# Performance work log

Measured on AMD Instinct MI355X. Metric: run time of the kernel, lower is better.

Reference implementation:

```python
import jax, jax.numpy as jnp
import numpy as np

CONTACT_THRESHOLD = 0.5
DEFAULT_LEN = 0.1
EPS = 1e-6


def _orthonormalize(m):
    # Gram-Schmidt on rows -> proper rotation matrices, vectorized over leading dims
    a1 = m[..., 0, :]
    a2 = m[..., 1, :]
    b1 = a1 / jnp.linalg.norm(a1, axis=-1, keepdims=True)
    a2p = a2 - jnp.sum(b1 * a2, axis=-1, keepdims=True) * b1
    b2 = a2p / jnp.linalg.norm(a2p, axis=-1, keepdims=True)
    b3 = jnp.cross(b1, b2)
    return jnp.stack([b1, b2, b3], axis=-2)


def setup_inputs() -> dict:
    key = jax.random.key(0)
    k1, k2, k3, k4 = jax.random.split(key, 4)
    B, T = 512, 4096
    pred_hand_contact_prob = jax.random.uniform(k1, (B, T, 2), dtype=jnp.float32)
    pred_hand_positions = jax.random.normal(k2, (B, T, 2, 3), dtype=jnp.float32)
    obj_rotm = _orthonormalize(jax.random.normal(k3, (B, T, 3, 3), dtype=jnp.float32))
    obj_trans_init = jax.random.normal(k4, (B, 3), dtype=jnp.float32)
    return {
        'pred_hand_contact_prob': pred_hand_contact_prob,
        'pred_hand_positions': pred_hand_positions,
        'obj_rotm': obj_rotm,
        'obj_trans_init': obj_trans_init,
    }


def _fk_obj_trans(contact_prob, hand_pos, obj_rotm, obj_trans_init):
    B, T, _ = contact_prob.shape
    dtype = hand_pos.dtype
    lc = contact_prob[..., 0] > CONTACT_THRESHOLD  # [B,T]
    rc = contact_prob[..., 1] > CONTACT_THRESHOLD
    t0 = jnp.zeros((B, 1), bool)  # frame 0 forced no-contact
    ls = jnp.concatenate([t0, lc[:, 1:] & ~lc[:, :-1]], axis=1)
    rs = jnp.concatenate([t0, rc[:, 1:] & ~rc[:, :-1]], axis=1)
    lc = jnp.concatenate([t0, lc[:, 1:]], axis=1)
    rc = jnp.concatenate([t0, rc[:, 1:]], axis=1)
    z_unit = jnp.array([0.0, 0.0, 1.0], dtype=dtype)
    bidx = jnp.arange(B)

    def step(carry, xs):
        current, obj_pos, dir_local, dist = carry  # [B] int32, [B,3], [B,3], [B]
        l_c, r_c, l_s, r_s, hands, R = xs  # hands [B,2,3], R [B,3,3]
        new = jnp.where(l_s, 0, jnp.where(r_s, 1, -1))
        has_contact = ((current == 0) & l_c) | ((current == 1) & r_c)
        has_other = ((current == 0) & r_c) | ((current == 1) & l_c)
        grab = (new != -1) | (~has_contact & has_other)
        cur_grab = jnp.where(new != -1, new, 1 - current)
        release = ~grab & ~has_contact & (current != -1)
        new_current = jnp.where(grab, cur_grab, jnp.where(release, -1, current))
        # grab: recompute local direction + distance from previous obj_pos
        hand0 = hands[bidx, jnp.clip(cur_grab, 0, 1)]  # [B,3]
        vec = obj_pos - hand0
        d0 = jnp.linalg.norm(vec, axis=-1)
        valid = d0 > EPS
        unit = jnp.where(valid[:, None], vec / jnp.maximum(d0, EPS)[:, None], z_unit)
        d0 = jnp.where(valid, d0, jnp.asarray(DEFAULT_LEN, dtype))
        dir_new = jnp.einsum('bij,bi->bj', R, unit)  # R^T @ unit
        dir_local = jnp.where(grab[:, None], dir_new, dir_local)
        dist = jnp.where(grab, d0, dist)
        # attached: obj_pos = hand + R @ dir_local * dist
        attached = new_current != -1
        hand_cur = hands[bidx, jnp.clip(new_current, 0, 1)]
        new_pos = hand_cur + jnp.einsum('bij,bj->bi', R, dir_local) * dist[:, None]
        obj_pos = jnp.where(attached[:, None], new_pos, obj_pos)
        return (new_current, obj_pos, dir_local, dist), obj_pos

    carry0 = (jnp.full((B,), -1, jnp.int32),
              obj_trans_init.astype(dtype),
              jnp.zeros((B, 3), dtype),
              jnp.zeros((B,), dtype))
    xs = (lc.T, rc.T, ls.T, rs.T,
          jnp.swapaxes(hand_pos, 0, 1),
          jnp.swapaxes(obj_rotm, 0, 1))
    _, out = jax.lax.scan(step, carry0, xs)  # out [T,B,3]
    return jnp.swapaxes(out, 0, 1)  # [B,T,3]


def reference(pred_hand_contact_prob, pred_hand_positions, obj_rotm, obj_trans_init):
    return _fk_obj_trans(pred_hand_contact_prob, pred_hand_positions, obj_rotm, obj_trans_init)
```

## Files before the change

### kernel.cpp

```cpp
#include <hip/hip_runtime.h>


#define FSM_ID 0x24

__device__ __forceinline__ int fsm_compose(int f, int g) {
    int r0 = (f >> (((g     ) & 3) << 1)) & 3;
    int r1 = (f >> (((g >> 2) & 3) << 1)) & 3;
    int r2 = (f >> (((g >> 4) & 3) << 1)) & 3;
    return r0 | (r1 << 2) | (r2 << 4);
}

__device__ __forceinline__ void tmap_identity(float* m, int& rp, int& rw) {
    #pragma unroll
    for (int i = 0; i < 24; ++i) m[i] = 0.f;
    m[0] = m[4] = m[8] = 1.f;
    m[12] = m[16] = m[20] = 1.f;
    rp = 0; rw = 1;
}

__device__ __forceinline__ void tmap_compose(
    const float* Lm, int Lrp, int Lrw,
    const float* Em, int Erp, int Erw,
    float* Om, int& Orp, int& Orw)
{
    {
        float EM[9], Ec[3];
        #pragma unroll
        for (int i = 0; i < 9; ++i) EM[i] = Lrp ? Em[12+i] : Em[i];
        #pragma unroll
        for (int i = 0; i < 3; ++i) Ec[i] = Lrp ? Em[21+i] : Em[9+i];
        #pragma unroll
        for (int i = 0; i < 3; ++i) {
            #pragma unroll
            for (int j = 0; j < 3; ++j)
                Om[3*i+j] = Lm[3*i]*EM[j] + Lm[3*i+1]*EM[3+j] + Lm[3*i+2]*EM[6+j];
            Om[9+i] = Lm[3*i]*Ec[0] + Lm[3*i+1]*Ec[1] + Lm[3*i+2]*Ec[2] + Lm[9+i];
        }
        Orp = Lrp ? Erw : Erp;
    }
    {
        float EM[9], Ec[3];
        #pragma unroll
        for (int i = 0; i < 9; ++i) EM[i] = Lrw ? Em[12+i] : Em[i];
        #pragma unroll
        for (int i = 0; i < 3; ++i) Ec[i] = Lrw ? Em[21+i] : Em[9+i];
        #pragma unroll
        for (int i = 0; i < 3; ++i) {
            #pragma unroll
            for (int j = 0; j < 3; ++j)
                Om[12+3*i+j] = Lm[12+3*i]*EM[j] + Lm[12+3*i+1]*EM[3+j] + Lm[12+3*i+2]*EM[6+j];
            Om[21+i] = Lm[12+3*i]*Ec[0] + Lm[12+3*i+1]*Ec[1] + Lm[12+3*i+2]*Ec[2] + Lm[21+i];
        }
        Orw = Lrw ? Erw : Erp;
    }
}

__device__ __forceinline__ void tmap_apply(
    const float* m, int rp_, int rw_,
    const float* pin, const float* win, float* pout, float* wout)
{
    const float* ip = rp_ ? win : pin;
    pout[0] = m[0]*ip[0] + m[1]*ip[1] + m[2]*ip[2] + m[9];
    pout[1] = m[3]*ip[0] + m[4]*ip[1] + m[5]*ip[2] + m[10];
    pout[2] = m[6]*ip[0] + m[7]*ip[1] + m[8]*ip[2] + m[11];
    const float* iw = rw_ ? win : pin;
    wout[0] = m[12]*iw[0] + m[13]*iw[1] + m[14]*iw[2] + m[21];
    wout[1] = m[15]*iw[0] + m[16]*iw[1] + m[17]*iw[2] + m[22];
    wout[2] = m[18]*iw[0] + m[19]*iw[1] + m[20]*iw[2] + m[23];
}

__global__ __launch_bounds__(1024) void fk_scan_par5(
    const float* __restrict__ prob,
    const float* __restrict__ hands,
    const float* __restrict__ rotm,
    const float* __restrict__ tinit,
    float* __restrict__ out)
{
    const int b    = blockIdx.x;
    const int c    = threadIdx.x;
    const int lane = c & 63;
    const int w    = c >> 6;

    __shared__ int   sFSM[16];
    __shared__ float sAm[16][24];
    __shared__ int   sAf[16];

    const float* prB = prob  + (size_t)b * 4096 * 2;
    const float* hdB = hands + (size_t)b * 4096 * 6;
    const float* rmB = rotm  + (size_t)b * 4096 * 9;
    float*       obB = out   + (size_t)b * 4096 * 3;

    const float4* pr4 = (const float4*)prB + c * 2;
    const float4* hd4 = (const float4*)hdB + c * 6;
    const float4* rm4 = (const float4*)rmB + c * 9;
    float4*       ob4 = (float4*)obB       + c * 3;

    unsigned lcB = 0, rcB = 0;
    #pragma unroll
    for (int i = 0; i < 2; ++i) {
        float4 v = pr4[i];
        lcB |= (unsigned)(v.x > 0.5f) << (2*i);
        rcB |= (unsigned)(v.y > 0.5f) << (2*i);
        lcB |= (unsigned)(v.z > 0.5f) << (2*i+1);
        rcB |= (unsigned)(v.w > 0.5f) << (2*i+1);
    }
    unsigned pL = 0, pR = 0;
    if (c) {
        float2 pv = *(const float2*)(prB + 8*c - 2);
        pL = pv.x > 0.5f ? 1u : 0u;
        pR = pv.y > 0.5f ? 1u : 0u;
    }
    unsigned lsB = lcB & ~((lcB << 1) | pL);
    unsigned rsB = rcB & ~((rcB << 1) | pR);
    if (c == 0) { lcB &= ~1u; rcB &= ~1u; lsB &= ~1u; rsB &= ~1u; }

    int M = FSM_ID;
    #pragma unroll
    for (int k = 0; k < 4; ++k) {
        const unsigned lc = (lcB >> k) & 1u, rc = (rcB >> k) & 1u;
        const unsigned ls = (lsB >> k) & 1u, rs = (rsB >> k) & 1u;
        const int nwi = (int)(ls | rs);
        const int nwe = ls ? 1 : 2;
        const int e0  = lc ? 1 : (rc ? 2 : 0);
        const int e1  = rc ? 2 : (lc ? 1 : 0);
        const int mt  = nwi ? nwe * 0x15 : ((e0 << 2) | (e1 << 4));
        M = fsm_compose(mt, M);
    }
    #pragma unroll
    for (int d = 1; d < 64; d <<= 1) {
        int v  = __shfl_up(M, d);
        int cc = fsm_compose(M, v);
        M = (lane >= d) ? cc : M;
    }
    if (lane == 63) sFSM[w] = M;
    __syncthreads();
    int Pf = FSM_ID;
    for (int i = 0; i < w; ++i) Pf = fsm_compose(sFSM[i], Pf);
    int Me = __shfl_up(M, 1);
    if (lane == 0) Me = FSM_ID;
    const int s_in = fsm_compose(Me, Pf) & 3;

    float Am[24]; int rp, rw;
    tmap_identity(Am, rp, rw);
    int s = s_in;
    {
        float rb[36], hb[24];
        #pragma unroll
        for (int j = 0; j < 9; ++j) {
            float4 v = rm4[j];
            rb[4*j]=v.x; rb[4*j+1]=v.y; rb[4*j+2]=v.z; rb[4*j+3]=v.w;
        }
        #pragma unroll
        for (int j = 0; j < 6; ++j) {
            float4 v = hd4[j];
            hb[4*j]=v.x; hb[4*j+1]=v.y; hb[4*j+2]=v.z; hb[4*j+3]=v.w;
        }
        #pragma unroll
        for (int k = 0; k < 4; ++k) {
            const unsigned lc=(lcB>>k)&1u, rc=(rcB>>k)&1u;
            const unsigned ls=(lsB>>k)&1u, rs=(rsB>>k)&1u;
            const int nwi  = (int)(ls|rs);
            const int c1 = (s==1), c2 = (s==2);
            const int hasc = (c1&(int)lc)|(c2&(int)rc);
            const int haso = (c1&(int)rc)|(c2&(int)lc);
            const int grab = nwi | ((hasc^1)&haso);
            const int gi   = nwi ? (ls?0:1) : c1;
            const int new_s= grab ? gi+1 : (hasc ? s : 0);
            const float* Rk = rb + 9*k;
            const float* Hk = hb + 6*k;
            if (grab) {
                const float hx = gi?Hk[3]:Hk[0], hy = gi?Hk[4]:Hk[1], hz = gi?Hk[5]:Hk[2];
                float t[9];
                #pragma unroll
                for (int i2=0;i2<3;++i2)
                    #pragma unroll
                    for (int j2=0;j2<3;++j2)
                        t[3*i2+j2] = Rk[i2]*Am[j2] + Rk[3+i2]*Am[3+j2] + Rk[6+i2]*Am[6+j2];
                const float ex=Am[9]-hx, ey=Am[10]-hy, ez=Am[11]-hz;
                Am[21] = Rk[0]*ex + Rk[3]*ey + Rk[6]*ez;
                Am[22] = Rk[1]*ex + Rk[4]*ey + Rk[7]*ez;
                Am[23] = Rk[2]*ex + Rk[5]*ey + Rk[8]*ez;
                #pragma unroll
                for (int i2=0;i2<9;++i2) Am[12+i2] = t[i2];
                rw = rp;
            } else if (new_s) {
                const int ci = new_s - 1;
                const float hx = ci?Hk[3]:Hk[0], hy = ci?Hk[4]:Hk[1], hz = ci?Hk[5]:Hk[2];
                float t[9];
                #pragma unroll
                for (int i2=0;i2<3;++i2)
                    #pragma unroll
                    for (int j2=0;j2<3;++j2)
                        t[3*i2+j2] = Rk[3*i2]*Am[12+j2] + Rk[3*i2+1]*Am[15+j2] + Rk[3*i2+2]*Am[18+j2];
                const float e0_ = hx + Rk[0]*Am[21] + Rk[1]*Am[22] + Rk[2]*Am[23];
                const float e1_ = hy + Rk[3]*Am[21] + Rk[4]*Am[22] + Rk[5]*Am[23];
                const float e2_ = hz + Rk[6]*Am[21] + Rk[7]*Am[22] + Rk[8]*Am[23];
                #pragma unroll
                for (int i2=0;i2<9;++i2) Am[i2] = t[i2];
                Am[9]=e0_; Am[10]=e1_; Am[11]=e2_;
                rp = rw;
            }
            s = new_s;
        }
    }

    #pragma unroll 1
    for (int d = 1; d < 64; d <<= 1) {
        float Em[24];
        #pragma unroll
        for (int i = 0; i < 24; ++i) Em[i] = __shfl_up(Am[i], d);
        const int Ef = __shfl_up(rp | (rw<<1), d);
        float Om[24]; int orp, orw;
        tmap_compose(Am, rp, rw, Em, Ef&1, (Ef>>1)&1, Om, orp, orw);
        const bool act = (lane >= d);
        #pragma unroll
        for (int i = 0; i < 24; ++i) Am[i] = act ? Om[i] : Am[i];
        rp = act ? orp : rp;
        rw = act ? orw : rw;
    }
    if (lane == 63) {
        #pragma unroll
        for (int i = 0; i < 24; ++i) sAm[w][i] = Am[i];
        sAf[w] = rp | (rw<<1);
    }
    __syncthreads();

    {
        #pragma unroll
        for (int i = 0; i < 24; ++i) Am[i] = __shfl_up(Am[i], 1);
        const int t = __shfl_up(rp | (rw<<1), 1);
        int nrp = t & 1, nrw = (t >> 1) & 1;
        if (lane == 0) tmap_identity(Am, nrp, nrw);
        rp = nrp; rw = nrw;
        if (lane == 0) { rp = 0; rw = 1; }
    }

    float vp[3] = { tinit[3*b], tinit[3*b+1], tinit[3*b+2] };
    float vw[3] = { 0.f, 0.f, 0.f };
    for (int i = 0; i < w; ++i) {
        float np[3], nw2[3];
        const int f = sAf[i];
        tmap_apply(&sAm[i][0], f & 1, (f >> 1) & 1, vp, vw, np, nw2);
        vp[0]=np[0]; vp[1]=np[1]; vp[2]=np[2];
        vw[0]=nw2[0]; vw[1]=nw2[1]; vw[2]=nw2[2];
    }
    float pv[3], wv[3];
    tmap_apply(Am, rp, rw, vp, vw, pv, wv);
    float px = pv[0], py = pv[1], pz = pv[2];
    float Wx = wv[0], Wy = wv[1], Wz = wv[2];

    s = s_in;
    {
        float rb[36], hb[24];
        #pragma unroll
        for (int j = 0; j < 9; ++j) {
            float4 v = rm4[j];
            rb[4*j]=v.x; rb[4*j+1]=v.y; rb[4*j+2]=v.z; rb[4*j+3]=v.w;
        }
        #pragma unroll
        for (int j = 0; j < 6; ++j) {
            float4 v = hd4[j];
            hb[4*j]=v.x; hb[4*j+1]=v.y; hb[4*j+2]=v.z; hb[4*j+3]=v.w;
        }
        float o[12];
        #pragma unroll
        for (int k = 0; k < 4; ++k) {
            const unsigned lc=(lcB>>k)&1u, rc=(rcB>>k)&1u;
            const unsigned ls=(lsB>>k)&1u, rs=(rsB>>k)&1u;
            const int nwi  = (int)(ls|rs);
            const int c1 = (s==1), c2 = (s==2);
            const int hasc = (c1&(int)lc)|(c2&(int)rc);
            const int haso = (c1&(int)rc)|(c2&(int)lc);
            const int grab = nwi | ((hasc^1)&haso);
            const int gi   = nwi ? (ls?0:1) : c1;
            const int new_s= grab ? gi+1 : (hasc ? s : 0);
            const float* Rk = rb + 9*k;
            const float* Hk = hb + 6*k;
            if (grab) {
                const float hx = gi?Hk[3]:Hk[0], hy = gi?Hk[4]:Hk[1], hz = gi?Hk[5]:Hk[2];
                const float vx = px-hx, vy = py-hy, vz = pz-hz;
                const float d2 = vx*vx + vy*vy + vz*vz;
                if (d2 > 1e-12f) {
                    Wx = Rk[0]*vx + Rk[3]*vy + Rk[6]*vz;
                    Wy = Rk[1]*vx + Rk[4]*vy + Rk[7]*vz;
                    Wz = Rk[2]*vx + Rk[5]*vy + Rk[8]*vz;
                } else {
                    Wx = 0.1f*Rk[6]; Wy = 0.1f*Rk[7]; Wz = 0.1f*Rk[8];
                }
            }
            if (new_s) {
                const int ci = new_s - 1;
                const float hx = ci?Hk[3]:Hk[0], hy = ci?Hk[4]:Hk[1], hz = ci?Hk[5]:Hk[2];
                px = hx + Rk[0]*Wx + Rk[1]*Wy + Rk[2]*Wz;
                py = hy + Rk[3]*Wx + Rk[4]*Wy + Rk[5]*Wz;
                pz = hz + Rk[6]*Wx + Rk[7]*Wy + Rk[8]*Wz;
            }
            s = new_s;
            o[3*k+0]=px; o[3*k+1]=py; o[3*k+2]=pz;
        }
        ob4[0] = make_float4(o[0], o[1], o[2],  o[3]);
        ob4[1] = make_float4(o[4], o[5], o[6],  o[7]);
        ob4[2] = make_float4(o[8], o[9], o[10], o[11]);
    }
}

#define CT 256
__global__ __launch_bounds__(64) void fk_scan_wave(
    const float* __restrict__ prob, const float* __restrict__ hands,
    const float* __restrict__ rotm, const float* __restrict__ tinit,
    float* __restrict__ out, int B, int T)
{
    __shared__ __align__(16) float sP[CT * 2];
    __shared__ __align__(16) float sH[CT * 8];
    __shared__ __align__(16) float sR[CT * 12];
    const int b = blockIdx.x, lane = threadIdx.x;
    const float* prB = prob  + (size_t)b * T * 2;
    const float* hdB = hands + (size_t)b * T * 6;
    const float* rmB = rotm  + (size_t)b * T * 9;
    float*       obB = out   + (size_t)b * T * 3;
    float px = tinit[3*b+0], py = tinit[3*b+1], pz = tinit[3*b+2];
    float Wx = 0.f, Wy = 0.f, Wz = 0.f;
    int cur = -1, prev_l = 0, prev_r = 0;
    for (int t0 = 0; t0 < T; t0 += CT) {
        const int n = (T - t0 < CT) ? (T - t0) : CT;
        for (int i = lane; i < n * 2; i += 64) sP[i] = prB[(size_t)t0*2 + i];
        for (int i = lane; i < n * 6; i += 64) {
            int s2 = i / 6, cc = i - 6*s2; sH[8*s2+cc] = hdB[(size_t)t0*6 + i];
        }
        for (int i = lane; i < n * 9; i += 64) {
            int s2 = i / 9, cc = i - 9*s2; sR[12*s2+cc] = rmB[(size_t)t0*9 + i];
        }
        __syncthreads();
        for (int k = 0; k < n; ++k) {
            const int t = t0 + k;
            const int rl = __builtin_amdgcn_readfirstlane(sP[2*k]   > 0.5f ? 1 : 0);
            const int rr = __builtin_amdgcn_readfirstlane(sP[2*k+1] > 0.5f ? 1 : 0);
            const int nz = (t != 0) ? 1 : 0;
            const int l_c = rl & nz, r_c = rr & nz;
            const int l_s = rl & (prev_l ^ 1) & nz, r_s = rr & (prev_r ^ 1) & nz;
            prev_l = rl; prev_r = rr;
            const int nw = l_s ? 0 : (r_s ? 1 : -1);
            const int hasc = ((cur==0)&l_c) | ((cur==1)&r_c);
            const int haso = ((cur==0)&r_c) | ((cur==1)&l_c);
            const int grab = (nw != -1) | ((hasc^1)&haso);
            const int new_cur = grab ? ((nw!=-1)?nw:(1-cur))
                                     : (((hasc^1)&(cur!=-1)) ? -1 : cur);
            if (new_cur != -1) {
                const float h0x=sH[8*k+0],h0y=sH[8*k+1],h0z=sH[8*k+2];
                const float h1x=sH[8*k+3],h1y=sH[8*k+4],h1z=sH[8*k+5];
                const float R0=sR[12*k+0],R1=sR[12*k+1],R2=sR[12*k+2];
                const float R3=sR[12*k+3],R4=sR[12*k+4],R5=sR[12*k+5];
                const float R6=sR[12*k+6],R7=sR[12*k+7],R8=sR[12*k+8];
                const float hx = new_cur ? h1x : h0x;
                const float hy = new_cur ? h1y : h0y;
                const float hz = new_cur ? h1z : h0z;
                if (grab) {
                    const float vx=px-hx, vy=py-hy, vz=pz-hz;
                    const float d2 = vx*vx+vy*vy+vz*vz;
                    if (d2 > 1e-12f) {
                        Wx = R0*vx+R3*vy+R6*vz; Wy = R1*vx+R4*vy+R7*vz; Wz = R2*vx+R5*vy+R8*vz;
                    } else { Wx = 0.1f*R6; Wy = 0.1f*R7; Wz = 0.1f*R8; }
                }
                px = hx + (R0*Wx+R1*Wy+R2*Wz);
                py = hy + (R3*Wx+R4*Wy+R5*Wz);
                pz = hz + (R6*Wx+R7*Wy+R8*Wz);
            }
            cur = new_cur;
            if (lane == 0) {
                obB[3*(size_t)t+0]=px; obB[3*(size_t)t+1]=py; obB[3*(size_t)t+2]=pz;
            }
        }
        __syncthreads();
    }
}

extern "C" void kernel_launch(void* const* d_in, const int* in_sizes, int n_in,
                              void* d_out, int out_size, void* d_ws, size_t ws_size,
                              hipStream_t stream) {
    const float* prob  = (const float*)d_in[0];
    const float* hands = (const float*)d_in[1];
    const float* rotm  = (const float*)d_in[2];
    const float* tinit = (const float*)d_in[3];
    float* out = (float*)d_out;

    const int B = in_sizes[3] / 3;
    const int T = in_sizes[0] / (B * 2);

    if (T == 4096) {
        hipLaunchKernelGGL(fk_scan_par5, dim3(B), dim3(1024), 0, stream,
                           prob, hands, rotm, tinit, out);
    } else {
        hipLaunchKernelGGL(fk_scan_wave, dim3(B), dim3(64), 0, stream,
                           prob, hands, rotm, tinit, out, B, T);
    }
}
```

Measured before the change: 61.71 us.

## Replace serial cross-wave prefix loops with a parallel 16-lane wave scan

The cross-wave carry for both the FSM state and the affine transform maps was previously built by each wave looping serially over all earlier waves' aggregates from shared memory. Now wave 0 runs a 16-lane shuffle scan over the wave aggregates once and writes per-wave starting states to shared memory, which every wave reads after an extra barrier. Each lane then applies its own inclusive map and takes the exclusive result via a shuffle. This removes up to 15 serial compose/apply steps per wave, in exchange for two extra __syncthreads and some register save/restore in wave 0.

```diff
diff --git a/kernel.cpp b/kernel.cpp
--- a/kernel.cpp
+++ b/kernel.cpp
@@ -69,7 +69,7 @@
     wout[2] = m[18]*iw[0] + m[19]*iw[1] + m[20]*iw[2] + m[23];
 }
 
-__global__ __launch_bounds__(1024) void fk_scan_par5(
+__global__ __launch_bounds__(1024) void fk_scan_par6(
     const float* __restrict__ prob,
     const float* __restrict__ hands,
     const float* __restrict__ rotm,
@@ -82,8 +82,12 @@
     const int w    = c >> 6;
 
     __shared__ int   sFSM[16];
+    __shared__ int   sSin[16];
     __shared__ float sAm[16][24];
     __shared__ int   sAf[16];
+    __shared__ float sSt[16][6];
+    __shared__ float sSave[16][24];
+    __shared__ int   sSvT[16];
 
     const float* prB = prob  + (size_t)b * 4096 * 2;
     const float* hdB = hands + (size_t)b * 4096 * 6;
@@ -134,11 +138,23 @@
     }
     if (lane == 63) sFSM[w] = M;
     __syncthreads();
-    int Pf = FSM_ID;
-    for (int i = 0; i < w; ++i) Pf = fsm_compose(sFSM[i], Pf);
+
+    if (w == 0 && lane < 16) {
+        int K = sFSM[lane];
+        #pragma unroll
+        for (int d = 1; d < 16; d <<= 1) {
+            int v  = __shfl_up(K, d);
+            int cc = fsm_compose(K, v);
+            K = (lane >= d) ? cc : K;
+        }
+        if (lane < 15) sSin[lane + 1] = K & 3;
+        if (lane == 0) sSin[0] = 0;
+    }
+    __syncthreads();
+
     int Me = __shfl_up(M, 1);
     if (lane == 0) Me = FSM_ID;
-    const int s_in = fsm_compose(Me, Pf) & 3;
+    const int s_in = (Me >> (2 * sSin[w])) & 3;
 
     float Am[24]; int rp, rw;
     tmap_identity(Am, rp, rw);
@@ -223,31 +239,63 @@
         for (int i = 0; i < 24; ++i) sAm[w][i] = Am[i];
         sAf[w] = rp | (rw<<1);
     }
+    if (w == 0 && lane < 16) {
+        #pragma unroll
+        for (int i = 0; i < 24; ++i) sSave[lane][i] = Am[i];
+        sSvT[lane] = rp | (rw<<1);
+    }
     __syncthreads();
 
-    {
-        #pragma unroll
-        for (int i = 0; i < 24; ++i) Am[i] = __shfl_up(Am[i], 1);
-        const int t = __shfl_up(rp | (rw<<1), 1);
-        int nrp = t & 1, nrw = (t >> 1) & 1;
-        if (lane == 0) tmap_identity(Am, nrp, nrw);
-        rp = nrp; rw = nrw;
-        if (lane == 0) { rp = 0; rw = 1; }
-    }
-
-    float vp[3] = { tinit[3*b], tinit[3*b+1], tinit[3*b+2] };
-    float vw[3] = { 0.f, 0.f, 0.f };
-    for (int i = 0; i < w; ++i) {
-        float np[3], nw2[3];
-        const int f = sAf[i];
-        tmap_apply(&sAm[i][0], f & 1, (f >> 1) & 1, vp, vw, np, nw2);
-        vp[0]=np[0]; vp[1]=np[1]; vp[2]=np[2];
-        vw[0]=nw2[0]; vw[1]=nw2[1]; vw[2]=nw2[2];
-    }
-    float pv[3], wv[3];
-    tmap_apply(Am, rp, rw, vp, vw, pv, wv);
-    float px = pv[0], py = pv[1], pz = pv[2];
-    float Wx = wv[0], Wy = wv[1], Wz = wv[2];
+    if (w == 0 && lane < 16) {
+        float Km[24];
+        #pragma unroll
+        for (int i = 0; i < 24; ++i) Km[i] = sAm[lane][i];
+        int kf = sAf[lane];
+        int krp = kf & 1, krw = (kf >> 1) & 1;
+        #pragma unroll 1
+        for (int d = 1; d < 16; d <<= 1) {
+            float Ek[24];
+            #pragma unroll
+            for (int i = 0; i < 24; ++i) Ek[i] = __shfl_up(Km[i], d);
+            const int Ef = __shfl_up(krp | (krw << 1), d);
+            float Ok[24]; int okp, okw;
+            tmap_compose(Km, krp, krw, Ek, Ef & 1, (Ef >> 1) & 1, Ok, okp, okw);
+            const bool act = (lane >= d);
+            #pragma unroll
+            for (int i = 0; i < 24; ++i) Km[i] = act ? Ok[i] : Km[i];
+            krp = act ? okp : krp;
+            krw = act ? okw : krw;
+        }
+        const float p0[3]  = { tinit[3*b], tinit[3*b+1], tinit[3*b+2] };
+        const float w0v[3] = { 0.f, 0.f, 0.f };
+        float sp[3], sw[3];
+        tmap_apply(Km, krp, krw, p0, w0v, sp, sw);
+        if (lane < 15) {
+            sSt[lane+1][0]=sp[0]; sSt[lane+1][1]=sp[1]; sSt[lane+1][2]=sp[2];
+            sSt[lane+1][3]=sw[0]; sSt[lane+1][4]=sw[1]; sSt[lane+1][5]=sw[2];
+        }
+        if (lane == 0) {
+            sSt[0][0]=p0[0]; sSt[0][1]=p0[1]; sSt[0][2]=p0[2];
+            sSt[0][3]=0.f;   sSt[0][4]=0.f;   sSt[0][5]=0.f;
+        }
+        #pragma unroll
+        for (int i = 0; i < 24; ++i) Am[i] = sSave[lane][i];
+        const int t2 = sSvT[lane];
+        rp = t2 & 1; rw = (t2 >> 1) & 1;
+    }
+    __syncthreads();
+
+    float vpv[3] = { sSt[w][0], sSt[w][1], sSt[w][2] };
+    float vwv[3] = { sSt[w][3], sSt[w][4], sSt[w][5] };
+    float ipv[3], iwv[3];
+    tmap_apply(Am, rp, rw, vpv, vwv, ipv, iwv);
+    float px = __shfl_up(ipv[0], 1);
+    float py = __shfl_up(ipv[1], 1);
+    float pz = __shfl_up(ipv[2], 1);
+    float Wx = __shfl_up(iwv[0], 1);
+    float Wy = __shfl_up(iwv[1], 1);
+    float Wz = __shfl_up(iwv[2], 1);
+    if (lane == 0) { px=vpv[0]; py=vpv[1]; pz=vpv[2]; Wx=vwv[0]; Wy=vwv[1]; Wz=vwv[2]; }
 
     s = s_in;
     {
@@ -387,7 +435,7 @@
     const int T = in_sizes[0] / (B * 2);
 
     if (T == 4096) {
-        hipLaunchKernelGGL(fk_scan_par5, dim3(B), dim3(1024), 0, stream,
+        hipLaunchKernelGGL(fk_scan_par6, dim3(B), dim3(1024), 0, stream,
                            prob, hands, rotm, tinit, out);
     } else {
         hipLaunchKernelGGL(fk_scan_wave, dim3(B), dim3(64), 0, stream,
```

New measurement: 63.95 us. 3.6% more time.

## Represent scan transform maps as quaternion plus translation in wave scan

Applied to the files above, without the earlier changes.

Each thread's local composed affine map, two 3x3 rotations plus offsets, is converted to a unit quaternion plus translation before the wave-level prefix scan. This cuts the per-step shuffle payload from 24 to 14 floats and uses cheaper quaternion products in place of 3x3 matrix multiplies. The exclusive-prefix step now shuffles the three-float applied result after applying the inclusive map, not the whole map. The trade-off is the cost of mat2quat conversions with branches and sqrt, plus rounding differences, and it assumes the composed matrices remain proper rotations.

```diff
diff --git a/kernel.cpp b/kernel.cpp
--- a/kernel.cpp
+++ b/kernel.cpp
@@ -10,66 +10,95 @@
     return r0 | (r1 << 2) | (r2 << 4);
 }
 
-__device__ __forceinline__ void tmap_identity(float* m, int& rp, int& rw) {
-    #pragma unroll
-    for (int i = 0; i < 24; ++i) m[i] = 0.f;
-    m[0] = m[4] = m[8] = 1.f;
-    m[12] = m[16] = m[20] = 1.f;
-    rp = 0; rw = 1;
-}
-
-__device__ __forceinline__ void tmap_compose(
-    const float* Lm, int Lrp, int Lrw,
-    const float* Em, int Erp, int Erw,
-    float* Om, int& Orp, int& Orw)
+__device__ __forceinline__ void qmul(const float* a, const float* b, float* o) {
+    o[0] = a[0]*b[0] - a[1]*b[1] - a[2]*b[2] - a[3]*b[3];
+    o[1] = a[0]*b[1] + a[1]*b[0] + a[2]*b[3] - a[3]*b[2];
+    o[2] = a[0]*b[2] - a[1]*b[3] + a[2]*b[0] + a[3]*b[1];
+    o[3] = a[0]*b[3] + a[1]*b[2] - a[2]*b[1] + a[3]*b[0];
+}
+
+__device__ __forceinline__ void qrot(const float* q, const float* v, float* o) {
+    const float ux = q[2]*v[2] - q[3]*v[1];
+    const float uy = q[3]*v[0] - q[1]*v[2];
+    const float uz = q[1]*v[1] - q[2]*v[0];
+    const float tx = ux + q[0]*v[0];
+    const float ty = uy + q[0]*v[1];
+    const float tz = uz + q[0]*v[2];
+    o[0] = fmaf(2.f, q[2]*tz - q[3]*ty, v[0]);
+    o[1] = fmaf(2.f, q[3]*tx - q[1]*tz, v[1]);
+    o[2] = fmaf(2.f, q[1]*ty - q[2]*tx, v[2]);
+}
+
+__device__ __forceinline__ void mat2quat(const float* m, float* q) {
+    const float tr = m[0] + m[4] + m[8];
+    float qw, qx, qy, qz;
+    if (tr > 0.f) {
+        const float S = sqrtf(tr + 1.0f) * 2.f, iS = 1.f / S;
+        qw = 0.25f * S;
+        qx = (m[7] - m[5]) * iS;
+        qy = (m[2] - m[6]) * iS;
+        qz = (m[3] - m[1]) * iS;
+    } else if (m[0] > m[4] && m[0] > m[8]) {
+        const float S = sqrtf(1.0f + m[0] - m[4] - m[8]) * 2.f, iS = 1.f / S;
+        qw = (m[7] - m[5]) * iS;
+        qx = 0.25f * S;
+        qy = (m[1] + m[3]) * iS;
+        qz = (m[2] + m[6]) * iS;
+    } else if (m[4] > m[8]) {
+        const float S = sqrtf(1.0f + m[4] - m[0] - m[8]) * 2.f, iS = 1.f / S;
+        qw = (m[2] - m[6]) * iS;
+        qx = (m[1] + m[3]) * iS;
+        qy = 0.25f * S;
+        qz = (m[5] + m[7]) * iS;
+    } else {
+        const float S = sqrtf(1.0f + m[8] - m[0] - m[4]) * 2.f, iS = 1.f / S;
+        qw = (m[3] - m[1]) * iS;
+        qx = (m[2] + m[6]) * iS;
+        qy = (m[5] + m[7]) * iS;
+        qz = 0.25f * S;
+    }
+    const float n = rsqrtf(qw*qw + qx*qx + qy*qy + qz*qz);
+    q[0] = qw*n; q[1] = qx*n; q[2] = qy*n; q[3] = qz*n;
+}
+
+__device__ __forceinline__ void qmap_compose(
+    const float* L, int Lrp, int Lrw,
+    const float* E, int Erp, int Erw,
+    float* O, int& Orp, int& Orw)
 {
-    {
-        float EM[9], Ec[3];
-        #pragma unroll
-        for (int i = 0; i < 9; ++i) EM[i] = Lrp ? Em[12+i] : Em[i];
-        #pragma unroll
-        for (int i = 0; i < 3; ++i) Ec[i] = Lrp ? Em[21+i] : Em[9+i];
-        #pragma unroll
-        for (int i = 0; i < 3; ++i) {
-            #pragma unroll
-            for (int j = 0; j < 3; ++j)
-                Om[3*i+j] = Lm[3*i]*EM[j] + Lm[3*i+1]*EM[3+j] + Lm[3*i+2]*EM[6+j];
-            Om[9+i] = Lm[3*i]*Ec[0] + Lm[3*i+1]*Ec[1] + Lm[3*i+2]*Ec[2] + Lm[9+i];
-        }
-        Orp = Lrp ? Erw : Erp;
-    }
-    {
-        float EM[9], Ec[3];
-        #pragma unroll
-        for (int i = 0; i < 9; ++i) EM[i] = Lrw ? Em[12+i] : Em[i];
-        #pragma unroll
-        for (int i = 0; i < 3; ++i) Ec[i] = Lrw ? Em[21+i] : Em[9+i];
-        #pragma unroll
-        for (int i = 0; i < 3; ++i) {
-            #pragma unroll
-            for (int j = 0; j < 3; ++j)
-                Om[12+3*i+j] = Lm[12+3*i]*EM[j] + Lm[12+3*i+1]*EM[3+j] + Lm[12+3*i+2]*EM[6+j];
-            Om[21+i] = Lm[12+3*i]*Ec[0] + Lm[12+3*i+1]*Ec[1] + Lm[12+3*i+2]*Ec[2] + Lm[21+i];
-        }
-        Orw = Lrw ? Erw : Erp;
-    }
-}
-
-__device__ __forceinline__ void tmap_apply(
+    float eq[4], ec[3], r[3];
+    #pragma unroll
+    for (int i = 0; i < 4; ++i) eq[i] = Lrp ? E[7+i] : E[i];
+    #pragma unroll
+    for (int i = 0; i < 3; ++i) ec[i] = Lrp ? E[11+i] : E[4+i];
+    qmul(L, eq, O);
+    qrot(L, ec, r);
+    O[4] = r[0] + L[4]; O[5] = r[1] + L[5]; O[6] = r[2] + L[6];
+    Orp = Lrp ? Erw : Erp;
+    #pragma unroll
+    for (int i = 0; i < 4; ++i) eq[i] = Lrw ? E[7+i] : E[i];
+    #pragma unroll
+    for (int i = 0; i < 3; ++i) ec[i] = Lrw ? E[11+i] : E[4+i];
+    qmul(L+7, eq, O+7);
+    qrot(L+7, ec, r);
+    O[11] = r[0] + L[11]; O[12] = r[1] + L[12]; O[13] = r[2] + L[13];
+    Orw = Lrw ? Erw : Erp;
+}
+
+__device__ __forceinline__ void qmap_apply(
     const float* m, int rp_, int rw_,
     const float* pin, const float* win, float* pout, float* wout)
 {
+    float r[3];
     const float* ip = rp_ ? win : pin;
-    pout[0] = m[0]*ip[0] + m[1]*ip[1] + m[2]*ip[2] + m[9];
-    pout[1] = m[3]*ip[0] + m[4]*ip[1] + m[5]*ip[2] + m[10];
-    pout[2] = m[6]*ip[0] + m[7]*ip[1] + m[8]*ip[2] + m[11];
+    qrot(m, ip, r);
+    pout[0] = r[0] + m[4]; pout[1] = r[1] + m[5]; pout[2] = r[2] + m[6];
     const float* iw = rw_ ? win : pin;
-    wout[0] = m[12]*iw[0] + m[13]*iw[1] + m[14]*iw[2] + m[21];
-    wout[1] = m[15]*iw[0] + m[16]*iw[1] + m[17]*iw[2] + m[22];
-    wout[2] = m[18]*iw[0] + m[19]*iw[1] + m[20]*iw[2] + m[23];
-}
-
-__global__ __launch_bounds__(1024) void fk_scan_par5(
+    qrot(m+7, iw, r);
+    wout[0] = r[0] + m[11]; wout[1] = r[1] + m[12]; wout[2] = r[2] + m[13];
+}
+
+__global__ __launch_bounds__(1024) void fk_scan_par9(
     const float* __restrict__ prob,
     const float* __restrict__ hands,
     const float* __restrict__ rotm,
@@ -82,8 +111,8 @@
     const int w    = c >> 6;
 
     __shared__ int   sFSM[16];
-    __shared__ float sAm[16][24];
-    __shared__ int   sAf[16];
+    __shared__ float sQ[16][14];
+    __shared__ int   sQf[16];
 
     const float* prB = prob  + (size_t)b * 4096 * 2;
     const float* hdB = hands + (size_t)b * 4096 * 6;
@@ -140,8 +169,11 @@
     if (lane == 0) Me = FSM_ID;
     const int s_in = fsm_compose(Me, Pf) & 3;
 
-    float Am[24]; int rp, rw;
-    tmap_identity(Am, rp, rw);
+    float Am[24]; int rp = 0, rw = 1;
+    #pragma unroll
+    for (int i = 0; i < 24; ++i) Am[i] = 0.f;
+    Am[0] = Am[4] = Am[8] = 1.f;
+    Am[12] = Am[16] = Am[20] = 1.f;
     int s = s_in;
     {
         float rb[36], hb[24];
@@ -204,50 +236,52 @@
         }
     }
 
+    float Qm[14];
+    mat2quat(Am, Qm);
+    Qm[4] = Am[9]; Qm[5] = Am[10]; Qm[6] = Am[11];
+    mat2quat(Am + 12, Qm + 7);
+    Qm[11] = Am[21]; Qm[12] = Am[22]; Qm[13] = Am[23];
+
     #pragma unroll 1
     for (int d = 1; d < 64; d <<= 1) {
-        float Em[24];
-        #pragma unroll
-        for (int i = 0; i < 24; ++i) Em[i] = __shfl_up(Am[i], d);
+        float Em[14];
+        #pragma unroll
+        for (int i = 0; i < 14; ++i) Em[i] = __shfl_up(Qm[i], d);
         const int Ef = __shfl_up(rp | (rw<<1), d);
-        float Om[24]; int orp, orw;
-        tmap_compose(Am, rp, rw, Em, Ef&1, (Ef>>1)&1, Om, orp, orw);
+        float Om[14]; int orp, orw;
+        qmap_compose(Qm, rp, rw, Em, Ef&1, (Ef>>1)&1, Om, orp, orw);
         const bool act = (lane >= d);
         #pragma unroll
-        for (int i = 0; i < 24; ++i) Am[i] = act ? Om[i] : Am[i];
+        for (int i = 0; i < 14; ++i) Qm[i] = act ? Om[i] : Qm[i];
         rp = act ? orp : rp;
         rw = act ? orw : rw;
     }
     if (lane == 63) {
         #pragma unroll
-        for (int i = 0; i < 24; ++i) sAm[w][i] = Am[i];
-        sAf[w] = rp | (rw<<1);
+        for (int i = 0; i < 14; ++i) sQ[w][i] = Qm[i];
+        sQf[w] = rp | (rw<<1);
     }
     __syncthreads();
-
-    {
-        #pragma unroll
-        for (int i = 0; i < 24; ++i) Am[i] = __shfl_up(Am[i], 1);
-        const int t = __shfl_up(rp | (rw<<1), 1);
-        int nrp = t & 1, nrw = (t >> 1) & 1;
-        if (lane == 0) tmap_identity(Am, nrp, nrw);
-        rp = nrp; rw = nrw;
-        if (lane == 0) { rp = 0; rw = 1; }
-    }
 
     float vp[3] = { tinit[3*b], tinit[3*b+1], tinit[3*b+2] };
     float vw[3] = { 0.f, 0.f, 0.f };
     for (int i = 0; i < w; ++i) {
         float np[3], nw2[3];
-        const int f = sAf[i];
-        tmap_apply(&sAm[i][0], f & 1, (f >> 1) & 1, vp, vw, np, nw2);
+        const int f = sQf[i];
+        qmap_apply(&sQ[i][0], f & 1, (f >> 1) & 1, vp, vw, np, nw2);
         vp[0]=np[0]; vp[1]=np[1]; vp[2]=np[2];
         vw[0]=nw2[0]; vw[1]=nw2[1]; vw[2]=nw2[2];
     }
-    float pv[3], wv[3];
-    tmap_apply(Am, rp, rw, vp, vw, pv, wv);
-    float px = pv[0], py = pv[1], pz = pv[2];
-    float Wx = wv[0], Wy = wv[1], Wz = wv[2];
+
+    float ipv[3], iwv[3];
+    qmap_apply(Qm, rp, rw, vp, vw, ipv, iwv);
+    float px = __shfl_up(ipv[0], 1);
+    float py = __shfl_up(ipv[1], 1);
+    float pz = __shfl_up(ipv[2], 1);
+    float Wx = __shfl_up(iwv[0], 1);
+    float Wy = __shfl_up(iwv[1], 1);
+    float Wz = __shfl_up(iwv[2], 1);
+    if (lane == 0) { px=vp[0]; py=vp[1]; pz=vp[2]; Wx=vw[0]; Wy=vw[1]; Wz=vw[2]; }
 
     s = s_in;
     {
@@ -387,7 +421,7 @@
     const int T = in_sizes[0] / (B * 2);
 
     if (T == 4096) {
-        hipLaunchKernelGGL(fk_scan_par5, dim3(B), dim3(1024), 0, stream,
+        hipLaunchKernelGGL(fk_scan_par9, dim3(B), dim3(1024), 0, stream,
                            prob, hands, rotm, tinit, out);
     } else {
         hipLaunchKernelGGL(fk_scan_wave, dim3(B), dim3(64), 0, stream,
```

Result: faster. 60.43 us, median of 2 (-2.1%).
